# Kernel optimization log

Hardware: AMD Instinct MI355X
Metric: run time of the kernel (lower is better)

The kernel has to match this reference:

```python
import jax, jax.numpy as jnp
import numpy as np

C = 256          # in_channels
CI = 128         # inter_channels = C // reduction
N_B, H, W = 4, 64, 64


def setup_inputs() -> dict:
    key = jax.random.key(0)
    ks = jax.random.split(key, 9)
    std = 0.01
    inp = {
        "x": jax.random.normal(ks[0], (N_B, C, H, W), dtype=jnp.float32),
        # 1x1 conv weights stored as [out_ch, in_ch]
        "w_g": jax.random.normal(ks[1], (CI, C), dtype=jnp.float32) * std,
        "b_g": jnp.zeros((CI,), dtype=jnp.float32),
        "w_theta": jax.random.normal(ks[2], (CI, C), dtype=jnp.float32) * std,
        "b_theta": jnp.zeros((CI,), dtype=jnp.float32),
        "w_phi": jax.random.normal(ks[3], (CI, C), dtype=jnp.float32) * std,
        "b_phi": jnp.zeros((CI,), dtype=jnp.float32),
        # conv_out: use small random instead of exact zeros so output is non-trivial
        "w_out": jax.random.normal(ks[4], (C, CI), dtype=jnp.float32) * std,
        "b_out": jnp.zeros((C,), dtype=jnp.float32),
    }
    return inp


def reference(x, w_g, b_g, w_theta, b_theta, w_phi, b_phi, w_out, b_out):
    n, c, h, w = x.shape
    nhw = h * w
    xf = x.reshape(n, c, nhw)                                   # [n, C, N]
    # 1x1 convs == channel matmuls
    g_x = jnp.einsum('ncs,oc->nso', xf, w_g) + b_g              # [n, N, CI]
    theta_x = jnp.einsum('ncs,oc->nso', xf, w_theta) + b_theta  # [n, N, CI]
    phi_x = jnp.einsum('ncs,oc->nos', xf, w_phi) + b_phi[None, :, None]  # [n, CI, N]
    # pairwise weights: [n, N, N]
    pw = jnp.einsum('nqc,ncs->nqs', theta_x, phi_x)
    # faithful to original: DIVIDE by d**-0.5 (i.e. multiply by sqrt(d))
    pw = pw / (theta_x.shape[-1] ** (-0.5))
    pw = jax.nn.softmax(pw, axis=-1)
    y = jnp.einsum('nqs,nsc->nqc', pw, g_x)                     # [n, N, CI]
    y = y.transpose(0, 2, 1).reshape(n, -1, h, w)               # [n, CI, H, W]
    out = jnp.einsum('nchw,oc->nohw', y, w_out) + b_out[None, :, None, None]
    return x + out
```

## Files before the change

kernel.cpp:

```cpp
#include <hip/hip_runtime.h>
#include <cmath>

typedef __attribute__((ext_vector_type(8))) short bf16x8;
typedef __attribute__((ext_vector_type(4))) float f32x4;
typedef __attribute__((ext_vector_type(16))) float f32x16;

#define MFMA16(a,b,c)  __builtin_amdgcn_mfma_f32_16x16x32_bf16((a),(b),(c),0,0,0)
#define MFMA32(a,b,c)  __builtin_amdgcn_mfma_f32_32x32x16_bf16((a),(b),(c),0,0,0)

#if __has_builtin(__builtin_amdgcn_exp2f)
#define EXP2F(x) __builtin_amdgcn_exp2f(x)
#else
#define EXP2F(x) exp2f(x)
#endif

#define KSCALE 16.3222312f

#define NB 4
#define CH 256
#define CI 128
#define NS 4096

__device__ __forceinline__ unsigned short f2bf(float f) {
    unsigned int u = __builtin_bit_cast(unsigned int, f);
    u += 0x7fffu + ((u >> 16) & 1u);
    return (unsigned short)(u >> 16);
}
__device__ __forceinline__ unsigned int pk2(float lo, float hi) {
    return (unsigned int)f2bf(lo) | ((unsigned int)f2bf(hi) << 16);
}
__device__ __forceinline__ unsigned int pkt(float lo, float hi) {
    return __builtin_amdgcn_perm(__builtin_bit_cast(unsigned int, hi),
                                 __builtin_bit_cast(unsigned int, lo), 0x07060302u);
}
__device__ __forceinline__ float bf2f(unsigned int ush) {
    return __builtin_bit_cast(float, ush << 16);
}

__device__ __forceinline__ void plswap(unsigned int& wLow, unsigned int& wHigh) {
    asm volatile("v_permlane32_swap_b32 %0, %1" : "+v"(wLow), "+v"(wHigh));
}

__device__ __forceinline__ f32x16 zero16() {
    f32x16 v;
#pragma unroll
    for (int i = 0; i < 16; i++) v[i] = 0.f;
    return v;
}

__device__ __forceinline__ void gload16(void* lds, const void* g) {
    __builtin_amdgcn_global_load_lds(
        (const __attribute__((address_space(1))) unsigned int*)g,
        (__attribute__((address_space(3))) unsigned int*)lds,
        16, 0, 0);
}

__global__ void wcvt_kernel(const float* __restrict__ w_g, const float* __restrict__ w_th,
                            const float* __restrict__ w_ph, const float* __restrict__ w_out,
                            const float* __restrict__ b_g, const float* __restrict__ b_th,
                            const float* __restrict__ b_ph,
                            unsigned short* __restrict__ wbf, float* __restrict__ bsc) {
    int i = blockIdx.x * 256 + threadIdx.x;
    float v;
    if (i < 98304) {
        int wi = i >> 15;
        int r  = i & 32767;
        int oh = r >> 14;
        int r2 = r & 16383;
        int kc = r2 >> 11;
        int r3 = r2 & 2047;
        int ot = r3 >> 9;
        int r4 = r3 & 511;
        int lane = r4 >> 3;
        int e  = r4 & 7;
        int o = oh * 64 + ot * 16 + (lane & 15);
        int c = kc * 32 + (lane >> 4) * 8 + e;
        const float* W = (wi == 0) ? w_g : (wi == 1 ? w_th : w_ph);
        v = W[o * CH + c];
        if (wi == 1) v *= KSCALE;
    } else {
        int r = i - 98304;
        int oh = r >> 14;
        int r2 = r & 16383;
        int kc = r2 >> 12;
        int r3 = r2 & 4095;
        int ot = r3 >> 9;
        int r4 = r3 & 511;
        int lane = r4 >> 3;
        int e = r4 & 7;
        int o = oh * 128 + ot * 16 + (lane & 15);
        int c = kc * 32 + (lane >> 4) * 8 + e;
        v = w_out[o * CI + c];
    }
    wbf[i] = f2bf(v);
    if (i < 128)          bsc[i] = b_g[i];
    else if (i < 256)     bsc[i] = b_th[i - 128] * KSCALE;
    else if (i < 384)     bsc[i] = b_ph[i - 256];
}

__global__ __launch_bounds__(512, 2)
void proj_kernel(const float* __restrict__ x,
                 const unsigned short* __restrict__ wbf, const float* __restrict__ bsc,
                 unsigned short* __restrict__ theta,
                 unsigned short* __restrict__ phi,
                 unsigned short* __restrict__ gT) {
    const int tid  = threadIdx.x;
    const int wid  = tid >> 6;
    const int lane = tid & 63;
    const int quad = lane >> 4;
    const int l15  = lane & 15;
    const int stile = blockIdx.x;
    const int n     = blockIdx.y;
    const int s0    = stile * 64;

    const float* xN = x + (size_t)n * CH * NS;

    __shared__ unsigned int xp[64 * 128];

#pragma unroll
    for (int i = 0; i < 4; i++) {
        int t  = i * 512 + tid;
        int s4 = t & 15;
        int cp = t >> 4;
        const float* p0 = xN + (size_t)(2 * cp) * NS + s0 + s4 * 4;
        float4 a = *(const float4*)p0;
        float4 b = *(const float4*)(p0 + NS);
        int col = (((cp >> 2) ^ (s4 & 7)) << 2) | (cp & 3);
        unsigned int* xr = xp + (s4 * 4) * 128 + col;
        xr[0]   = pk2(a.x, b.x);
        xr[128] = pk2(a.y, b.y);
        xr[256] = pk2(a.z, b.z);
        xr[384] = pk2(a.w, b.w);
    }
    __syncthreads();

    const int srow = (wid & 3) * 16 + l15;
    const int oh   = wid >> 2;
    const int sw7  = (srow >> 2) & 7;
#pragma unroll
    for (int wi = 0; wi < 3; wi++) {
        f32x4 acc[4];
#pragma unroll
        for (int ot = 0; ot < 4; ot++) acc[ot] = (f32x4){0.f, 0.f, 0.f, 0.f};
        const unsigned short* W = wbf + (size_t)(wi * 2 + oh) * 16384;
#pragma unroll
        for (int kc = 0; kc < 8; kc++) {
            bf16x8 af = *(const bf16x8*)(&xp[srow * 128 + (((kc * 4 + quad) ^ sw7) << 2)]);
#pragma unroll
            for (int ot = 0; ot < 4; ot++) {
                bf16x8 wf = *(const bf16x8*)(W + kc * 2048 + ot * 512 + lane * 8);
                acc[ot] = MFMA16(af, wf, acc[ot]);
            }
        }
        const float* Bv = bsc + wi * 128 + oh * 64;
#pragma unroll
        for (int ot = 0; ot < 4; ot++) {
            int o = oh * 64 + ot * 16 + l15;
            float bias = Bv[ot * 16 + l15];
            if (wi == 0) {
                int sg0 = s0 + (wid & 3) * 16 + quad * 4;
                uint2 w;
                w.x = pk2(acc[ot][0] + bias, acc[ot][1] + bias);
                w.y = pk2(acc[ot][2] + bias, acc[ot][3] + bias);
                *(uint2*)(gT + (size_t)((size_t)n * CI + o) * NS + sg0) = w;
            } else {
#pragma unroll
                for (int r = 0; r < 4; r++) {
                    int sg = s0 + (wid & 3) * 16 + quad * 4 + r;
                    float v = acc[ot][r] + bias;
                    if (wi == 1)
                        theta[((size_t)n * NS + sg) * CI + o] = f2bf(v);
                    else
                        phi[((size_t)n * NS + sg) * CI + o] = f2bf(v);
                }
            }
        }
    }
}

__global__ __launch_bounds__(256, 2)
void attn_kernel(const unsigned short* __restrict__ theta,
                 const unsigned short* __restrict__ phi,
                 const unsigned short* __restrict__ gT,
                 unsigned short* __restrict__ Opart,
                 float* __restrict__ lbuf) {
    const int tid  = threadIdx.x;
    const int wid  = tid >> 6;
    const int lane = tid & 63;
    const int l31  = lane & 31;
    const int lh32 = lane >> 5;
    const int sn    = blockIdx.x;
    const int split = sn >> 2;
    const int n     = sn & 3;
    const int qb    = blockIdx.y;
    const int qbase = qb * 128 + wid * 32;

    const unsigned short* thN = theta + (size_t)n * NS * CI;
    const unsigned short* phN = phi   + (size_t)n * NS * CI;
    const unsigned short* gN  = gT    + (size_t)n * CI * NS;

    __shared__ unsigned short smem[32768];
    unsigned short* Kb = smem;
    unsigned short* Vb = smem + 16384;

    bf16x8 qf[8];
#pragma unroll
    for (int kc = 0; kc < 8; kc++)
        qf[kc] = *(const bf16x8*)(thN + (size_t)(qbase + l31) * CI + kc * 16 + lh32 * 8);

    f32x16 O[4];
#pragma unroll
    for (int ct = 0; ct < 4; ct++) O[ct] = zero16();
    float lrun = 0.f;

    const int sbase0 = split * 1024;
    const int lh16 = lane >> 4, lm16 = lane & 15;
    const int lh8  = lane >> 3, lm8  = lane & 7;

#pragma unroll
    for (int i = 0; i < 4; i++) {
        int seg = wid * 4 + i;
        int s   = seg * 4 + lh16;
        int j   = lm16 ^ (s & 15);
        gload16(Kb + seg * 512, phN + (size_t)(sbase0 + s) * CI + j * 8);
    }
#pragma unroll
    for (int i = 0; i < 4; i++) {
        int seg = wid * 4 + i;
        int c   = seg * 8 + lh8;
        int j   = lm8 ^ (c & 7);
        gload16(Vb + seg * 512, gN + (size_t)c * NS + sbase0 + j * 8);
    }

    for (int ck = 0; ck < 16; ck++) {
        const int cur = ck & 1, nxt = cur ^ 1;
        unsigned short* Kc = Kb + cur * 8192;
        unsigned short* Vc = Vb + cur * 8192;
        __syncthreads();

        if (ck + 1 < 16) {
            const int sb1 = sbase0 + (ck + 1) * 64;
#pragma unroll
            for (int i = 0; i < 4; i++) {
                int seg = wid * 4 + i;
                int s   = seg * 4 + lh16;
                int j   = lm16 ^ (s & 15);
                gload16(Kb + nxt * 8192 + seg * 512, phN + (size_t)(sb1 + s) * CI + j * 8);
            }
#pragma unroll
            for (int i = 0; i < 4; i++) {
                int seg = wid * 4 + i;
                int c   = seg * 8 + lh8;
                int j   = lm8 ^ (c & 7);
                gload16(Vb + nxt * 8192 + seg * 512, gN + (size_t)c * NS + sb1 + j * 8);
            }
        }

        f32x16 S[2];
        S[0] = zero16(); S[1] = zero16();
        __builtin_amdgcn_s_setprio(1);
#pragma unroll
        for (int sb = 0; sb < 2; sb++) {
#pragma unroll
            for (int kc = 0; kc < 8; kc++) {
                int s = sb * 32 + l31;
                bf16x8 kf = *(const bf16x8*)(Kc + s * 128 + (((kc * 2 + lh32) ^ (s & 15)) * 8));
                S[sb] = MFMA32(kf, qf[kc], S[sb]);
            }
        }
        __builtin_amdgcn_s_setprio(0);

        bf16x8 pf[4];
        float lsum = 0.f;
#pragma unroll
        for (int ks = 0; ks < 4; ks++) {
            const int sb = ks >> 1, b = ks & 1;
            float pA[4], pB[4];
#pragma unroll
            for (int m = 0; m < 4; m++) {
                pA[m] = EXP2F(S[sb][(2 * b) * 4 + m]);
                pB[m] = EXP2F(S[sb][(2 * b + 1) * 4 + m]);
            }
            lsum += ((pA[0] + pA[1]) + (pA[2] + pA[3]))
                  + ((pB[0] + pB[1]) + (pB[2] + pB[3]));
            unsigned int wA0 = pkt(pA[0], pA[1]);
            unsigned int wA1 = pkt(pA[2], pA[3]);
            unsigned int wB0 = pkt(pB[0], pB[1]);
            unsigned int wB1 = pkt(pB[2], pB[3]);
            plswap(wA0, wB0);
            plswap(wA1, wB1);
            union { unsigned int u[4]; bf16x8 v; } P;
            P.u[0] = wA0; P.u[1] = wA1; P.u[2] = wB0; P.u[3] = wB1;
            pf[ks] = P.v;
        }
        lrun += lsum;

        __builtin_amdgcn_s_setprio(1);
#pragma unroll
        for (int ks = 0; ks < 4; ks++) {
#pragma unroll
            for (int ct = 0; ct < 4; ct++) {
                int c = ct * 32 + l31;
                bf16x8 vf = *(const bf16x8*)(Vc + c * 64 + (((ks * 2 + lh32) ^ (c & 7)) * 8));
                O[ct] = MFMA32(vf, pf[ks], O[ct]);
            }
        }
        __builtin_amdgcn_s_setprio(0);
    }

    __syncthreads();
    float* tb = (float*)smem + wid * 2048;
    const size_t obase = ((size_t)(split * NB + n)) * NS * CI;
#pragma unroll
    for (int pass = 0; pass < 2; pass++) {
#pragma unroll
        for (int cti = 0; cti < 2; cti++) {
            const int ct = pass * 2 + cti;
#pragma unroll
            for (int g = 0; g < 4; g++) {
                const int c_local = cti * 32 + 8 * g + 4 * lh32;
                const int slot = (c_local >> 2) ^ (l31 & 15);
                f32x4 v;
                v[0] = O[ct][4 * g + 0]; v[1] = O[ct][4 * g + 1];
                v[2] = O[ct][4 * g + 2]; v[3] = O[ct][4 * g + 3];
                *(f32x4*)(tb + l31 * 64 + slot * 4) = v;
            }
        }
#pragma unroll
        for (int i = 0; i < 8; i++) {
            const int qr  = i * 4 + (lane >> 4);
            const int lin = lane & 15;
            f32x4 v = *(const f32x4*)(tb + qr * 64 + ((lin ^ (qr & 15)) * 4));
            uint2 w;
            w.x = pk2(v[0], v[1]);
            w.y = pk2(v[2], v[3]);
            *(uint2*)(Opart + obase + (size_t)(qbase + qr) * CI + pass * 64 + lin * 4) = w;
        }
    }
    lrun += __shfl_xor(lrun, 32);
    if (lane < 32)
        lbuf[(split * NB + n) * NS + qbase + l31] = lrun;
}

__global__ __launch_bounds__(256, 4)
void outproj_kernel(const float* __restrict__ x,
                    const unsigned short* __restrict__ wbf,
                    const float* __restrict__ b_out,
                    const unsigned short* __restrict__ Opart,
                    const float* __restrict__ lbuf,
                    float* __restrict__ out) {
    const int tid  = threadIdx.x;
    const int wid  = tid >> 6;
    const int lane = tid & 63;
    const int quad = lane >> 4;
    const int l15  = lane & 15;
    const int oh = blockIdx.y;
    const int n  = blockIdx.z;
    const int sw = blockIdx.x * 64 + wid * 16;
    const int T  = NB * NS;

    const int srow = n * NS + sw + l15;
    float l = 0.f;
#pragma unroll
    for (int k = 0; k < 4; k++) l += lbuf[k * T + srow];
    float rinv = 1.0f / l;

    bf16x8 yb[4];
#pragma unroll
    for (int kc = 0; kc < 4; kc++) {
        float f0 = 0.f, f1 = 0.f, f2 = 0.f, f3 = 0.f;
        float f4 = 0.f, f5 = 0.f, f6 = 0.f, f7 = 0.f;
#pragma unroll
        for (int k = 0; k < 4; k++) {
            uint4 v = *(const uint4*)(Opart + ((size_t)k * T + srow) * CI + kc * 32 + quad * 8);
            f0 += bf2f(v.x & 0xffffu); f1 += bf2f(v.x >> 16);
            f2 += bf2f(v.y & 0xffffu); f3 += bf2f(v.y >> 16);
            f4 += bf2f(v.z & 0xffffu); f5 += bf2f(v.z >> 16);
            f6 += bf2f(v.w & 0xffffu); f7 += bf2f(v.w >> 16);
        }
        union { unsigned int uu[4]; bf16x8 vv; } r;
        r.uu[0] = pk2(f0 * rinv, f1 * rinv);
        r.uu[1] = pk2(f2 * rinv, f3 * rinv);
        r.uu[2] = pk2(f4 * rinv, f5 * rinv);
        r.uu[3] = pk2(f6 * rinv, f7 * rinv);
        yb[kc] = r.vv;
    }

    const unsigned short* wof = wbf + 98304 + (size_t)oh * 16384;
    f32x4 acc[8];
#pragma unroll
    for (int ot = 0; ot < 8; ot++) acc[ot] = (f32x4){0.f, 0.f, 0.f, 0.f};
#pragma unroll
    for (int kc = 0; kc < 4; kc++) {
#pragma unroll
        for (int ot = 0; ot < 8; ot++) {
            bf16x8 wa = *(const bf16x8*)(wof + kc * 4096 + ot * 512 + lane * 8);
            acc[ot] = MFMA16(wa, yb[kc], acc[ot]);
        }
    }
#pragma unroll
    for (int ot = 0; ot < 8; ot++) {
#pragma unroll
        for (int r = 0; r < 4; r++) {
            int o = oh * 128 + ot * 16 + quad * 4 + r;
            size_t idx = ((size_t)n * CH + o) * NS + sw + l15;
            out[idx] = x[idx] + acc[ot][r] + b_out[o];
        }
    }
}

extern "C" void kernel_launch(void* const* d_in, const int* in_sizes, int n_in,
                              void* d_out, int out_size, void* d_ws, size_t ws_size,
                              hipStream_t stream) {
    const float* x     = (const float*)d_in[0];
    const float* w_g   = (const float*)d_in[1];
    const float* b_g   = (const float*)d_in[2];
    const float* w_th  = (const float*)d_in[3];
    const float* b_th  = (const float*)d_in[4];
    const float* w_ph  = (const float*)d_in[5];
    const float* b_ph  = (const float*)d_in[6];
    const float* w_out = (const float*)d_in[7];
    const float* b_out = (const float*)d_in[8];
    float* out = (float*)d_out;

    char* ws = (char*)d_ws;
    unsigned short* theta = (unsigned short*)(ws + 0);
    unsigned short* phi   = (unsigned short*)(ws + 4194304);
    unsigned short* gT    = (unsigned short*)(ws + 8388608);
    unsigned short* Opart = (unsigned short*)(ws + 12582912);
    float* lbuf  = (float*)(ws + 29360128);
    unsigned short* wbf = (unsigned short*)(ws + 29622272);
    float* bsc   = (float*)(ws + 29884416);

    wcvt_kernel<<<512, 256, 0, stream>>>(w_g, w_th, w_ph, w_out, b_g, b_th, b_ph, wbf, bsc);
    proj_kernel<<<dim3(64, NB), 512, 0, stream>>>(x, wbf, bsc, theta, phi, gT);
    attn_kernel<<<dim3(16, 32), 256, 0, stream>>>(theta, phi, gT, Opart, lbuf);
    outproj_kernel<<<dim3(64, 2, NB), 256, 0, stream>>>(x, wbf, b_out, Opart, lbuf, out);
}
```

Baseline: 144.3 us.

## Coalesce theta/phi stores via swapped MFMA operands; stage Opart through LDS

The projection kernel swaps the MFMA operand order for theta and phi so each lane holds four consecutive output channels. Those results can then be written as packed 8-byte stores instead of scattered 2-byte stores. The output-projection kernel loads the four partial attention outputs into a swizzled 64KB shared buffer using gload16 and reduces them from LDS, replacing strided global reads. The added shared memory forces launch bounds to 2 blocks per CU, which lowers occupancy.

```diff
diff --git a/kernel.cpp b/kernel.cpp
--- a/kernel.cpp
+++ b/kernel.cpp
@@ -149,30 +149,32 @@
 #pragma unroll
             for (int ot = 0; ot < 4; ot++) {
                 bf16x8 wf = *(const bf16x8*)(W + kc * 2048 + ot * 512 + lane * 8);
-                acc[ot] = MFMA16(af, wf, acc[ot]);
+                if (wi == 0) acc[ot] = MFMA16(af, wf, acc[ot]);
+                else         acc[ot] = MFMA16(wf, af, acc[ot]);
             }
         }
         const float* Bv = bsc + wi * 128 + oh * 64;
-#pragma unroll
-        for (int ot = 0; ot < 4; ot++) {
-            int o = oh * 64 + ot * 16 + l15;
-            float bias = Bv[ot * 16 + l15];
-            if (wi == 0) {
+        if (wi == 0) {
+#pragma unroll
+            for (int ot = 0; ot < 4; ot++) {
+                int o = oh * 64 + ot * 16 + l15;
+                float bias = Bv[ot * 16 + l15];
                 int sg0 = s0 + (wid & 3) * 16 + quad * 4;
                 uint2 w;
                 w.x = pk2(acc[ot][0] + bias, acc[ot][1] + bias);
                 w.y = pk2(acc[ot][2] + bias, acc[ot][3] + bias);
                 *(uint2*)(gT + (size_t)((size_t)n * CI + o) * NS + sg0) = w;
-            } else {
-#pragma unroll
-                for (int r = 0; r < 4; r++) {
-                    int sg = s0 + (wid & 3) * 16 + quad * 4 + r;
-                    float v = acc[ot][r] + bias;
-                    if (wi == 1)
-                        theta[((size_t)n * NS + sg) * CI + o] = f2bf(v);
-                    else
-                        phi[((size_t)n * NS + sg) * CI + o] = f2bf(v);
-                }
+            }
+        } else {
+            unsigned short* dst = (wi == 1) ? theta : phi;
+            const int sgl = s0 + srow;
+#pragma unroll
+            for (int ot = 0; ot < 4; ot++) {
+                f32x4 bb = *(const f32x4*)(Bv + ot * 16 + quad * 4);
+                uint2 w;
+                w.x = pk2(acc[ot][0] + bb[0], acc[ot][1] + bb[1]);
+                w.y = pk2(acc[ot][2] + bb[2], acc[ot][3] + bb[3]);
+                *(uint2*)(dst + ((size_t)n * NS + sgl) * CI + oh * 64 + ot * 16 + quad * 4) = w;
             }
         }
     }
@@ -342,7 +344,7 @@
         lbuf[(split * NB + n) * NS + qbase + l31] = lrun;
 }
 
-__global__ __launch_bounds__(256, 4)
+__global__ __launch_bounds__(256, 2)
 void outproj_kernel(const float* __restrict__ x,
                     const unsigned short* __restrict__ wbf,
                     const float* __restrict__ b_out,
@@ -356,8 +358,24 @@
     const int l15  = lane & 15;
     const int oh = blockIdx.y;
     const int n  = blockIdx.z;
-    const int sw = blockIdx.x * 64 + wid * 16;
+    const int s0 = blockIdx.x * 64;
+    const int sw = s0 + wid * 16;
     const int T  = NB * NS;
+
+    __shared__ unsigned short Ob[4 * 64 * 128];
+
+    const int lh16 = lane >> 4, lm16 = lane & 15;
+#pragma unroll
+    for (int k = 0; k < 4; k++) {
+#pragma unroll
+        for (int i = 0; i < 4; i++) {
+            int seg = wid * 4 + i;
+            int s   = seg * 4 + lh16;
+            int j   = lm16 ^ (s & 15);
+            gload16(Ob + k * 8192 + seg * 512,
+                    Opart + ((size_t)k * T + (size_t)n * NS + s0 + s) * CI + j * 8);
+        }
+    }
 
     const int srow = n * NS + sw + l15;
     float l = 0.f;
@@ -365,14 +383,18 @@
     for (int k = 0; k < 4; k++) l += lbuf[k * T + srow];
     float rinv = 1.0f / l;
 
+    __syncthreads();
+
+    const int sL = wid * 16 + l15;
     bf16x8 yb[4];
 #pragma unroll
     for (int kc = 0; kc < 4; kc++) {
         float f0 = 0.f, f1 = 0.f, f2 = 0.f, f3 = 0.f;
         float f4 = 0.f, f5 = 0.f, f6 = 0.f, f7 = 0.f;
+        const int slot = (kc * 4 + quad) ^ (sL & 15);
 #pragma unroll
         for (int k = 0; k < 4; k++) {
-            uint4 v = *(const uint4*)(Opart + ((size_t)k * T + srow) * CI + kc * 32 + quad * 8);
+            uint4 v = *(const uint4*)(Ob + k * 8192 + sL * 128 + slot * 8);
             f0 += bf2f(v.x & 0xffffu); f1 += bf2f(v.x >> 16);
             f2 += bf2f(v.y & 0xffffu); f3 += bf2f(v.y >> 16);
             f4 += bf2f(v.z & 0xffffu); f5 += bf2f(v.z >> 16);
```

Result: no change. 146.7 us (+1.7%).
